# Kernel tuning notes

Measured on AMD Instinct MI355X. Metric: run time of the kernel, lower is better.

## Reference

```python
import jax, jax.numpy as jnp
import numpy as np

N_NODES = 100000
N_EDGES = 3200000
M = 24
HID = 32
OUT = 16


def neighbor_mean(feat, row, col, num_nodes):
    # sum features of source nodes into destination nodes, divide by in-degree
    sums = jax.ops.segment_sum(feat[row], col, num_segments=num_nodes)  # (N, F)
    deg = jax.ops.segment_sum(jnp.ones_like(col, dtype=feat.dtype), col, num_segments=num_nodes)
    return sums / jnp.clip(deg, 1.0)[:, None]


def sage_conv(x, row, col, num_nodes, w_l, b_l, w_r):
    # PyG SAGEConv(aggr='mean'): lin_l(mean_aggr) + lin_r(x); lin_r has no bias
    aggr = neighbor_mean(x, row, col, num_nodes)
    return aggr @ w_l.T + b_l + x @ w_r.T


def setup_inputs() -> dict:
    key = jax.random.key(0)
    ks = jax.random.split(key, 10)
    x_bin = jax.random.randint(ks[0], (N_NODES, M), 0, 2).astype(jnp.float32)
    edge_index = jax.random.randint(ks[1], (2, N_EDGES), 0, N_NODES).astype(jnp.int64)
    s = 0.1
    return {
        "x_bin": x_bin,
        "edge_index": edge_index,
        "w1l": s * jax.random.normal(ks[2], (HID, M), jnp.float32),
        "b1": s * jax.random.normal(ks[3], (HID,), jnp.float32),
        "w1r": s * jax.random.normal(ks[4], (HID, M), jnp.float32),
        "w2l": s * jax.random.normal(ks[5], (OUT, HID), jnp.float32),
        "b2": s * jax.random.normal(ks[6], (OUT,), jnp.float32),
        "w2r": s * jax.random.normal(ks[7], (OUT, HID), jnp.float32),
        "head_w": s * jax.random.normal(ks[8], (1, 3 * M + OUT), jnp.float32),
        "head_b": s * jax.random.normal(ks[9], (1,), jnp.float32),
    }


def reference(x_bin, edge_index, w1l, b1, w1r, w2l, b2, w2r, head_w, head_b):
    num_nodes = x_bin.shape[0]
    row, col = edge_index[0], edge_index[1]
    # explicit branch: [self markers | neighbor fraction | self * neighbor fraction]
    frac1 = neighbor_mean(x_bin, row, col, num_nodes)
    feats = jnp.concatenate([x_bin, frac1, x_bin * frac1], axis=1)  # (N, 3M)
    # GNN branch: SmallSAGE (dropout is identity at inference)
    h = jax.nn.relu(sage_conv(x_bin, row, col, num_nodes, w1l, b1, w1r))
    emb = jax.nn.relu(sage_conv(h, row, col, num_nodes, w2l, b2, w2r))  # (N, OUT)
    z = jnp.concatenate([feats, emb], axis=1)  # (N, 3M+OUT)
    yhat = (z @ head_w.T + head_b)[:, 0]  # (N,)
    return yhat, z
```

## Files before the change

### kernel.cpp

```cpp
#include <hip/hip_runtime.h>
#include <hip/hip_bf16.h>

#define MF 24
#define HIDF 32
#define OUTF 16
#define ZDIM 88
#define NPB 8
#define NPB2 32
#define SW1 28
#define SW2 36

#define NB 512
#define EB 8192
#define CAP 8192

union bf16x8 {
    float4 v;
    __hip_bfloat16 h[8];
};
union bf16x2u {
    unsigned int u;
    __hip_bfloat16 h[2];
};

__device__ __forceinline__ float ldw(const void* p, size_t i, bool bf16) {
    return bf16 ? __bfloat162float(((const __hip_bfloat16*)p)[i])
                : ((const float*)p)[i];
}

__device__ __forceinline__ bool detect_bf(const unsigned int* __restrict__ xw) {
    unsigned int w = xw[threadIdx.x & 63];
    return __ballot((w & 0xFFFFu) == 0x3F80u) != 0ull;
}
__device__ __forceinline__ bool detect_i64(const unsigned int* __restrict__ ew) {
    unsigned int w = ew[2 * (threadIdx.x & 63) + 1];
    return __popcll(__ballot(w == 0u)) >= 32;
}

__global__ __launch_bounds__(256) void k_histA(
    const void* __restrict__ x, unsigned int* __restrict__ xpack,
    const int* __restrict__ ei, int* __restrict__ counts,
    int nE, int N, int W) {
    const bool bf16 = detect_bf((const unsigned int*)x);
    const bool i64 = detect_i64((const unsigned int*)ei);

    for (int n = blockIdx.x * 256 + threadIdx.x; n < N; n += gridDim.x * 256) {
        unsigned int m = 0;
        if (bf16) {
            const float4* xr = reinterpret_cast<const float4*>(
                (const __hip_bfloat16*)x + (size_t)n * MF);
            bf16x8 u;
#pragma unroll
            for (int q = 0; q < 3; ++q) {
                u.v = xr[q];
#pragma unroll
                for (int i = 0; i < 8; ++i)
                    if (__bfloat162float(u.h[i]) != 0.f) m |= 1u << (q * 8 + i);
            }
        } else {
            const float* xr = (const float*)x + (size_t)n * MF;
#pragma unroll
            for (int k = 0; k < MF; ++k)
                if (xr[k] != 0.f) m |= 1u << k;
        }
        xpack[n] = m;
    }

    __shared__ int hist[NB];
    for (int i = threadIdx.x; i < NB; i += 256) hist[i] = 0;
    __syncthreads();
    size_t base = (size_t)blockIdx.x * EB;
    int m = nE - (int)base;
    if (m > EB) m = EB;
    for (int i = threadIdx.x; i < m; i += 256) {
        size_t e = base + i;
        int c = i64 ? ei[2 * ((size_t)nE + e)] : ei[(size_t)nE + e];
        if ((unsigned)c < (unsigned)N) atomicAdd(&hist[c / W], 1);
    }
    __syncthreads();
    for (int i = threadIdx.x; i < NB; i += 256)
        counts[(size_t)blockIdx.x * NB + i] = hist[i];
}

__global__ __launch_bounds__(1024) void k_colscan(int* __restrict__ counts,
                                                  int* __restrict__ colSum, int nBlk) {
    __shared__ int s[1024];
    int b = blockIdx.x, t = threadIdx.x;
    int v = (t < nBlk) ? counts[(size_t)t * NB + b] : 0;
    s[t] = v;
    __syncthreads();
    for (int off = 1; off < 1024; off <<= 1) {
        int y = (t >= off) ? s[t - off] : 0;
        __syncthreads();
        s[t] += y;
        __syncthreads();
    }
    if (t < nBlk) counts[(size_t)t * NB + b] = s[t] - v;
    if (t == 1023) colSum[b] = s[1023];
}

__global__ __launch_bounds__(1024) void k_bstart(const int* __restrict__ colSum,
                                                 int* __restrict__ bucketStart) {
    __shared__ int s[1024];
    int t = threadIdx.x;
    int v = (t < NB) ? colSum[t] : 0;
    s[t] = v;
    __syncthreads();
    for (int off = 1; off < 1024; off <<= 1) {
        int y = (t >= off) ? s[t - off] : 0;
        __syncthreads();
        s[t] += y;
        __syncthreads();
    }
    if (t < NB) bucketStart[t] = s[t] - v;
    if (t == NB - 1) bucketStart[NB] = s[t];
}

__global__ __launch_bounds__(256) void k_scatB(
    const int* __restrict__ ei, const int* __restrict__ counts,
    const int* __restrict__ colSum, const int* __restrict__ bucketStart,
    unsigned int* __restrict__ part, int nE, int N, int W, int nBlk) {
    const bool i64 = detect_i64((const unsigned int*)ei);
    __shared__ unsigned int rec[EB];
    __shared__ unsigned short bkt[EB];
    __shared__ int ldsStart[NB + 1];
    __shared__ int lcnt[NB];
    __shared__ int base2[NB];
    __shared__ int s256[256];
    const int t = threadIdx.x, blk = blockIdx.x;

    for (int b = t; b < NB; b += 256) {
        int pre = counts[(size_t)blk * NB + b];
        int nxt = (blk + 1 < nBlk) ? counts[(size_t)(blk + 1) * NB + b] : colSum[b];
        ldsStart[b] = nxt - pre;
        lcnt[b] = 0;
        base2[b] = bucketStart[b] + pre;
    }
    __syncthreads();

    int v0 = ldsStart[2 * t], v1 = ldsStart[2 * t + 1];
    int pairSum = v0 + v1;
    s256[t] = pairSum;
    __syncthreads();
    for (int off = 1; off < 256; off <<= 1) {
        int y = (t >= off) ? s256[t - off] : 0;
        __syncthreads();
        s256[t] += y;
        __syncthreads();
    }
    int base = s256[t] - pairSum;
    ldsStart[2 * t] = base;
    ldsStart[2 * t + 1] = base + v0;
    if (t == 255) ldsStart[NB] = base + pairSum;
    __syncthreads();
    for (int b = t; b < NB; b += 256) base2[b] -= ldsStart[b];
    __syncthreads();

    size_t eb = (size_t)blk * EB;
    int m = nE - (int)eb;
    if (m > EB) m = EB;
    for (int i = t; i < m; i += 256) {
        size_t e = eb + i;
        int r = i64 ? ei[2 * e] : ei[e];
        int c = i64 ? ei[2 * ((size_t)nE + e)] : ei[(size_t)nE + e];
        if ((unsigned)c < (unsigned)N) {
            int b = c / W;
            int ld = c - b * W;
            unsigned rr = ((unsigned)r < (unsigned)N) ? (unsigned)r : 0u;
            int pos = ldsStart[b] + atomicAdd(&lcnt[b], 1);
            rec[pos] = rr | ((unsigned)ld << 20);
            bkt[pos] = (unsigned short)b;
        }
    }
    __syncthreads();

    int total = ldsStart[NB];
    for (int i = t; i < total; i += 256) {
        int b = bkt[i];
        part[base2[b] + i] = rec[i];
    }
}

__global__ __launch_bounds__(256) void k_csrC(const int* __restrict__ bucketStart,
                                              unsigned int* __restrict__ part,
                                              int* __restrict__ degi,
                                              int* __restrict__ rowstart,
                                              int N, int W) {
    __shared__ unsigned int stage[CAP];
    __shared__ int hist[256];
    __shared__ int sc[256];
    __shared__ int cur[256];
    int b = blockIdx.x, t = threadIdx.x;
    int start = bucketStart[b];
    int bs = bucketStart[b + 1] - start;
    int node = b * W + t;

    hist[t] = 0;
    __syncthreads();

    if (bs > CAP) {
        if (t < W && node < N) { degi[node] = 0; rowstart[node] = start; }
        return;
    }

    for (int i = t; i < bs; i += 256) {
        unsigned int v = part[start + i];
        stage[i] = v;
        atomicAdd(&hist[v >> 20], 1);
    }
    __syncthreads();

    int v = hist[t];
    sc[t] = v;
    __syncthreads();
    for (int off = 1; off < 256; off <<= 1) {
        int y = (t >= off) ? sc[t - off] : 0;
        __syncthreads();
        sc[t] += y;
        __syncthreads();
    }
    int excl = sc[t] - v;
    if (t < W && node < N) {
        degi[node] = v;
        rowstart[node] = start + excl;
    }
    cur[t] = excl;
    __syncthreads();

    for (int i = t; i < bs; i += 256) {
        unsigned int v2 = stage[i];
        int pos = atomicAdd(&cur[v2 >> 20], 1);
        part[start + pos] = v2 & 0xFFFFFu;
    }
}

__device__ __forceinline__ unsigned tstage(unsigned x, unsigned y, unsigned M,
                                           int d, bool hi) {
    return x ^ (hi ? (((y >> d) ^ x) & M) : (((((x >> d) ^ y) & M)) << d));
}

__device__ __forceinline__ unsigned tcol(unsigned x, int lane) {
    unsigned y;
    y = (unsigned)__builtin_amdgcn_ds_swizzle((int)x, 0x401F);
    x = tstage(x, y, 0x0000FFFFu, 16, (lane & 16) != 0);
    y = (unsigned)__builtin_amdgcn_ds_swizzle((int)x, 0x201F);
    x = tstage(x, y, 0x00FF00FFu, 8, (lane & 8) != 0);
    y = (unsigned)__builtin_amdgcn_ds_swizzle((int)x, 0x101F);
    x = tstage(x, y, 0x0F0F0F0Fu, 4, (lane & 4) != 0);
    y = (unsigned)__builtin_amdgcn_ds_swizzle((int)x, 0x081F);
    x = tstage(x, y, 0x33333333u, 2, (lane & 2) != 0);
    y = (unsigned)__builtin_amdgcn_ds_swizzle((int)x, 0x041F);
    x = tstage(x, y, 0x55555555u, 1, (lane & 1) != 0);
    return x;
}

__global__ __launch_bounds__(256) void k_layer1(
    const void* __restrict__ x, const unsigned int* __restrict__ xpack,
    const int* __restrict__ degi, const int* __restrict__ rowstart,
    const unsigned int* __restrict__ srcs, void* __restrict__ out,
    const void* __restrict__ w1l, const void* __restrict__ b1,
    const void* __restrict__ w1r, const void* __restrict__ w2l,
    const void* __restrict__ b2, const void* __restrict__ w2r,
    const void* __restrict__ head_w,
    __hip_bfloat16* __restrict__ hl, __hip_bfloat16* __restrict__ st,
    float* __restrict__ ypart, int N) {
    const bool bf16 = detect_bf((const unsigned int*)x);
    __shared__ float swl[HIDF * SW1];
    __shared__ float swr[HIDF * SW1];
    __shared__ float sb[HIDF];
    __shared__ float s2l[OUTF * SW2];
    __shared__ float s2r[OUTF * SW2];
    __shared__ float sb2[OUTF];
    __shared__ float shw[3 * MF];
    __shared__ float fs[NPB][MF];
    __shared__ float hs[NPB][HIDF];
    for (int i = threadIdx.x; i < HIDF * MF; i += 256) {
        int j = i / MF, k = i - j * MF;
        swl[j * SW1 + k] = ldw(w1l, i, bf16);
        swr[j * SW1 + k] = ldw(w1r, i, bf16);
    }
    for (int i = threadIdx.x; i < OUTF * HIDF; i += 256) {
        int o = i >> 5, j = i & 31;
        s2l[o * SW2 + j] = ldw(w2l, i, bf16);
        s2r[o * SW2 + j] = ldw(w2r, i, bf16);
    }
    if (threadIdx.x < HIDF) sb[threadIdx.x] = ldw(b1, threadIdx.x, bf16);
    if (threadIdx.x < OUTF) sb2[threadIdx.x] = ldw(b2, threadIdx.x, bf16);
    if (threadIdx.x < 3 * MF) shw[threadIdx.x] = ldw(head_w, threadIdx.x, bf16);
    __syncthreads();

    const int lane = threadIdx.x & 31;
    const int wg = threadIdx.x >> 5;
    int node = blockIdx.x * NPB + wg;
    bool valid = node < N;

    int dg = 0, p0 = 0;
    unsigned int xpn = 0;
    if (valid) {
        dg = degi[node];
        p0 = rowstart[node];
        xpn = xpack[node];
    }

    int dgmax = dg;
#pragma unroll
    for (int off = 32; off > 0; off >>= 1)
        dgmax = max(dgmax, __shfl_xor(dgmax, off, 64));

    int cnt = 0;
    for (int base = 0; base < dgmax; base += 128) {
        unsigned int m0 = 0, m1 = 0, m2 = 0, m3 = 0;
        int e0 = base + lane;
        if (e0 < dg) m0 = xpack[srcs[p0 + e0]];
        if (e0 + 32 < dg) m1 = xpack[srcs[p0 + e0 + 32]];
        if (e0 + 64 < dg) m2 = xpack[srcs[p0 + e0 + 64]];
        if (e0 + 96 < dg) m3 = xpack[srcs[p0 + e0 + 96]];
        cnt += __popc(tcol(m0, lane));
        if (base + 32 < dgmax) cnt += __popc(tcol(m1, lane));
        if (base + 64 < dgmax) cnt += __popc(tcol(m2, lane));
        if (base + 96 < dgmax) cnt += __popc(tcol(m3, lane));
    }

    float inv = 1.f / fmaxf((float)dg, 1.f);
    float fv = (float)cnt * inv;
    float xv = (float)((xpn >> lane) & 1);

    float pc = 0.f;
    if (valid && lane < MF) {
        if (bf16) {
            __hip_bfloat16* z = (__hip_bfloat16*)out + N + (size_t)node * ZDIM;
            z[lane] = __float2bfloat16(xv);
            z[MF + lane] = __float2bfloat16(fv);
            z[2 * MF + lane] = __float2bfloat16(xv * fv);
        } else {
            float* z = (float*)out + N + (size_t)node * ZDIM;
            z[lane] = xv;
            z[MF + lane] = fv;
            z[2 * MF + lane] = xv * fv;
        }
        pc = xv * shw[lane] + fv * shw[MF + lane] + xv * fv * shw[2 * MF + lane];
    }

    if (lane < MF) fs[wg][lane] = fv;

    float fvk[MF];
    {
        const float4* fp = (const float4*)fs[wg];
#pragma unroll
        for (int q = 0; q < 6; ++q) {
            float4 f4 = fp[q];
            fvk[q * 4 + 0] = f4.x; fvk[q * 4 + 1] = f4.y;
            fvk[q * 4 + 2] = f4.z; fvk[q * 4 + 3] = f4.w;
        }
    }
    float wlv[MF], wrv[MF];
    {
        const float4* wl4 = (const float4*)(swl + lane * SW1);
        const float4* wr4 = (const float4*)(swr + lane * SW1);
#pragma unroll
        for (int q = 0; q < 6; ++q) {
            float4 a = wl4[q], b = wr4[q];
            wlv[q * 4 + 0] = a.x; wlv[q * 4 + 1] = a.y;
            wlv[q * 4 + 2] = a.z; wlv[q * 4 + 3] = a.w;
            wrv[q * 4 + 0] = b.x; wrv[q * 4 + 1] = b.y;
            wrv[q * 4 + 2] = b.z; wrv[q * 4 + 3] = b.w;
        }
    }
    float acc = sb[lane];
#pragma unroll
    for (int k = 0; k < MF; ++k) {
        acc = fmaf(fvk[k], wlv[k], acc);
        acc += ((xpn >> k) & 1u) ? wrv[k] : 0.f;
    }
    hs[wg][lane] = fmaxf(acc, 0.f);

#pragma unroll
    for (int off = 16; off > 0; off >>= 1) pc += __shfl_down(pc, off, 32);

    int o = lane & 15;
    int half = lane >> 4;
    const float4* wrow4 = (const float4*)((half ? s2r : s2l) + o * SW2);
    const float4* hp4 = (const float4*)hs[wg];
    float d = 0.f;
#pragma unroll
    for (int q = 0; q < 8; ++q) {
        float4 hq = hp4[q], wq = wrow4[q];
        d += hq.x * wq.x + hq.y * wq.y + hq.z * wq.z + hq.w * wq.w;
    }
    if (valid) {
        if (half == 0) hl[(size_t)node * OUTF + o] = __float2bfloat16(d);
        else st[(size_t)node * OUTF + o] = __float2bfloat16(d + sb2[o]);
        if (lane == 0) ypart[node] = pc;
    }
}

__global__ __launch_bounds__(256) void k_layer2(
    const void* __restrict__ x, const int* __restrict__ degi,
    const int* __restrict__ rowstart, const unsigned int* __restrict__ srcs,
    const __hip_bfloat16* __restrict__ hl, const __hip_bfloat16* __restrict__ st,
    const float* __restrict__ ypart, void* __restrict__ out,
    const void* __restrict__ head_w, const void* __restrict__ head_b, int N) {
    const bool bf16 = detect_bf((const unsigned int*)x);
    __shared__ float shw2[OUTF];
    __shared__ float shb;
    if (threadIdx.x < OUTF) shw2[threadIdx.x] = ldw(head_w, 3 * MF + threadIdx.x, bf16);
    if (threadIdx.x == 0) shb = ldw(head_b, 0, bf16);
    __syncthreads();

    int lane = threadIdx.x & 7;
    int g = threadIdx.x >> 3;
    int node = blockIdx.x * NPB2 + g;
    bool valid = node < N;

    int dg = 0, p0 = 0;
    if (valid) {
        dg = degi[node];
        p0 = rowstart[node];
    }
    const unsigned int* hlw = (const unsigned int*)hl;
    float s0 = 0.f, s1 = 0.f;
    int e = 0;
    for (; e + 4 <= dg; e += 4) {
        int a = srcs[p0 + e], b = srcs[p0 + e + 1];
        int c = srcs[p0 + e + 2], d = srcs[p0 + e + 3];
        bf16x2u ua, ub, uc, ud;
        ua.u = hlw[(size_t)a * 8 + lane];
        ub.u = hlw[(size_t)b * 8 + lane];
        uc.u = hlw[(size_t)c * 8 + lane];
        ud.u = hlw[(size_t)d * 8 + lane];
        s0 += (__bfloat162float(ua.h[0]) + __bfloat162float(ub.h[0])) +
              (__bfloat162float(uc.h[0]) + __bfloat162float(ud.h[0]));
        s1 += (__bfloat162float(ua.h[1]) + __bfloat162float(ub.h[1])) +
              (__bfloat162float(uc.h[1]) + __bfloat162float(ud.h[1]));
    }
    for (; e < dg; ++e) {
        bf16x2u ua;
        ua.u = hlw[(size_t)srcs[p0 + e] * 8 + lane];
        s0 += __bfloat162float(ua.h[0]);
        s1 += __bfloat162float(ua.h[1]);
    }

    float emb0 = 0.f, emb1 = 0.f;
    if (valid) {
        float inv = 1.f / fmaxf((float)dg, 1.f);
        bf16x2u us;
        us.u = ((const unsigned int*)st)[(size_t)node * 8 + lane];
        emb0 = fmaxf(s0 * inv + __bfloat162float(us.h[0]), 0.f);
        emb1 = fmaxf(s1 * inv + __bfloat162float(us.h[1]), 0.f);
        if (bf16) {
            __hip_bfloat16* z = (__hip_bfloat16*)out + N + (size_t)node * ZDIM;
            z[3 * MF + 2 * lane] = __float2bfloat16(emb0);
            z[3 * MF + 2 * lane + 1] = __float2bfloat16(emb1);
        } else {
            float* z = (float*)out + N + (size_t)node * ZDIM;
            z[3 * MF + 2 * lane] = emb0;
            z[3 * MF + 2 * lane + 1] = emb1;
        }
    }
    float part = emb0 * shw2[2 * lane] + emb1 * shw2[2 * lane + 1];
#pragma unroll
    for (int off = 4; off > 0; off >>= 1) part += __shfl_down(part, off, 8);
    if (valid && lane == 0) {
        float y = ypart[node] + part + shb;
        if (bf16) ((__hip_bfloat16*)out)[node] = __float2bfloat16(y);
        else ((float*)out)[node] = y;
    }
}

extern "C" void kernel_launch(void* const* d_in, const int* in_sizes, int n_in,
                              void* d_out, int out_size, void* d_ws, size_t ws_size,
                              hipStream_t stream) {
    const void* x = d_in[0];
    const int* ei = (const int*)d_in[1];
    const void* w1l = d_in[2];
    const void* b1 = d_in[3];
    const void* w1r = d_in[4];
    const void* w2l = d_in[5];
    const void* b2 = d_in[6];
    const void* w2r = d_in[7];
    const void* head_w = d_in[8];
    const void* head_b = d_in[9];

    const int N = in_sizes[0] / MF;
    const int nE = in_sizes[1] / 2;
    const int W = (N + NB - 1) / NB;
    const int nBlkA = (nE + EB - 1) / EB;

    if (N > NB * 256 || N > 131072 || nBlkA > 1024 ||
        (size_t)nBlkA * NB < (size_t)N || nE < 64) return;

    int* bucketStart = (int*)((char*)d_ws + 256);
    int* colSum = bucketStart + (NB + 1);
    int* degi = colSum + NB;
    int* rowstart = degi + N;
    int* counts = rowstart + N;
    unsigned int* part = (unsigned int*)(counts + (size_t)nBlkA * NB);
    unsigned int* xpack = part + nE;
    __hip_bfloat16* hl = (__hip_bfloat16*)(xpack + N);
    __hip_bfloat16* st = hl + (size_t)N * OUTF;
    float* ypart = (float*)counts;

    const size_t need = 256 +
        ((size_t)(NB + 1) + NB + 2 * (size_t)N + (size_t)nBlkA * NB +
         (size_t)nE + (size_t)N) * 4 + (size_t)N * OUTF * 2 * 2;
    if (ws_size < need) return;

    const int gb1 = (N + NPB - 1) / NPB;
    const int gb2 = (N + NPB2 - 1) / NPB2;
    k_histA<<<nBlkA, 256, 0, stream>>>(x, xpack, ei, counts, nE, N, W);
    k_colscan<<<NB, 1024, 0, stream>>>(counts, colSum, nBlkA);
    k_bstart<<<1, 1024, 0, stream>>>(colSum, bucketStart);
    k_scatB<<<nBlkA, 256, 0, stream>>>(ei, counts, colSum, bucketStart,
                                       part, nE, N, W, nBlkA);
    k_csrC<<<NB, 256, 0, stream>>>(bucketStart, part, degi, rowstart, N, W);
    k_layer1<<<gb1, 256, 0, stream>>>(x, xpack, degi, rowstart, part, d_out,
                                      w1l, b1, w1r, w2l, b2, w2r, head_w,
                                      hl, st, ypart, N);
    k_layer2<<<gb2, 256, 0, stream>>>(x, degi, rowstart, part, hl, st, ypart,
                                      d_out, head_w, head_b, N);
}
```

Before: 256.1 us.

## Vectorize edge loads, use reciprocal bucket division, halve edge block, loop layer1 nodes

The histogram and scatter kernels now load edge indices two at a time with int2/int4 vector loads and compute bucket indices with a multiply-high reciprocal instead of an integer divide. The edge block size drops from 8192 to 4096, doubling the number of partition blocks and the size of the counts array. k_layer1 now handles two node groups per block in a loop, which halves its grid and amortizes the weight staging into LDS. Together these aim to cut the overhead of the CSR build and the layer-1 setup, at the cost of more colscan work and fewer layer-1 blocks in flight.

```diff
diff --git a/kernel.cpp b/kernel.cpp
--- a/kernel.cpp
+++ b/kernel.cpp
@@ -6,12 +6,13 @@
 #define OUTF 16
 #define ZDIM 88
 #define NPB 8
+#define NREP 2
 #define NPB2 32
 #define SW1 28
 #define SW2 36
 
 #define NB 512
-#define EB 8192
+#define EB 4096
 #define CAP 8192
 
 union bf16x8 {
@@ -37,10 +38,17 @@
     return __popcll(__ballot(w == 0u)) >= 32;
 }
 
+__device__ __forceinline__ int bkt_of(int c, unsigned long long Wm) {
+    return (int)(((unsigned long long)(unsigned)c * Wm) >> 32);
+}
+
+#define HIST_EDGE(c_)                                                   \
+    if ((unsigned)(c_) < (unsigned)N) atomicAdd(&hist[bkt_of(c_, Wm)], 1);
+
 __global__ __launch_bounds__(256) void k_histA(
     const void* __restrict__ x, unsigned int* __restrict__ xpack,
     const int* __restrict__ ei, int* __restrict__ counts,
-    int nE, int N, int W) {
+    int nE, int N, unsigned long long Wm) {
     const bool bf16 = detect_bf((const unsigned int*)x);
     const bool i64 = detect_i64((const unsigned int*)ei);
 
@@ -72,10 +80,34 @@
     size_t base = (size_t)blockIdx.x * EB;
     int m = nE - (int)base;
     if (m > EB) m = EB;
-    for (int i = threadIdx.x; i < m; i += 256) {
-        size_t e = base + i;
-        int c = i64 ? ei[2 * ((size_t)nE + e)] : ei[(size_t)nE + e];
-        if ((unsigned)c < (unsigned)N) atomicAdd(&hist[c / W], 1);
+    if (!(nE & 1)) {
+        int nPair = m >> 1;
+        if (i64) {
+            const int4* cp = (const int4*)ei + (((size_t)nE + base) >> 1);
+            for (int j = threadIdx.x; j < nPair; j += 256) {
+                int4 c4 = cp[j];
+                HIST_EDGE(c4.x);
+                HIST_EDGE(c4.z);
+            }
+        } else {
+            const int2* cp = (const int2*)ei + (((size_t)nE + base) >> 1);
+            for (int j = threadIdx.x; j < nPair; j += 256) {
+                int2 c2 = cp[j];
+                HIST_EDGE(c2.x);
+                HIST_EDGE(c2.y);
+            }
+        }
+        for (int i = (nPair << 1) + threadIdx.x; i < m; i += 256) {
+            size_t e = base + i;
+            int c = i64 ? ei[2 * ((size_t)nE + e)] : ei[(size_t)nE + e];
+            HIST_EDGE(c);
+        }
+    } else {
+        for (int i = threadIdx.x; i < m; i += 256) {
+            size_t e = base + i;
+            int c = i64 ? ei[2 * ((size_t)nE + e)] : ei[(size_t)nE + e];
+            HIST_EDGE(c);
+        }
     }
     __syncthreads();
     for (int i = threadIdx.x; i < NB; i += 256)
@@ -116,10 +148,21 @@
     if (t == NB - 1) bucketStart[NB] = s[t];
 }
 
+#define SCAT_EDGE(r_, c_)                                               \
+    if ((unsigned)(c_) < (unsigned)N) {                                 \
+        int b_ = bkt_of(c_, Wm);                                        \
+        int ld_ = (c_) - b_ * W;                                        \
+        unsigned rr_ = ((unsigned)(r_) < (unsigned)N) ? (unsigned)(r_) : 0u; \
+        int pos_ = ldsStart[b_] + atomicAdd(&lcnt[b_], 1);              \
+        rec[pos_] = rr_ | ((unsigned)ld_ << 20);                        \
+        bkt[pos_] = (unsigned short)b_;                                 \
+    }
+
 __global__ __launch_bounds__(256) void k_scatB(
     const int* __restrict__ ei, const int* __restrict__ counts,
     const int* __restrict__ colSum, const int* __restrict__ bucketStart,
-    unsigned int* __restrict__ part, int nE, int N, int W, int nBlk) {
+    unsigned int* __restrict__ part, int nE, int N, int W,
+    unsigned long long Wm, int nBlk) {
     const bool i64 = detect_i64((const unsigned int*)ei);
     __shared__ unsigned int rec[EB];
     __shared__ unsigned short bkt[EB];
@@ -159,17 +202,39 @@
     size_t eb = (size_t)blk * EB;
     int m = nE - (int)eb;
     if (m > EB) m = EB;
-    for (int i = t; i < m; i += 256) {
-        size_t e = eb + i;
-        int r = i64 ? ei[2 * e] : ei[e];
-        int c = i64 ? ei[2 * ((size_t)nE + e)] : ei[(size_t)nE + e];
-        if ((unsigned)c < (unsigned)N) {
-            int b = c / W;
-            int ld = c - b * W;
-            unsigned rr = ((unsigned)r < (unsigned)N) ? (unsigned)r : 0u;
-            int pos = ldsStart[b] + atomicAdd(&lcnt[b], 1);
-            rec[pos] = rr | ((unsigned)ld << 20);
-            bkt[pos] = (unsigned short)b;
+    if (!(nE & 1)) {
+        int nPair = m >> 1;
+        if (i64) {
+            const int4* rp = (const int4*)ei + (eb >> 1);
+            const int4* cp = (const int4*)ei + (((size_t)nE + eb) >> 1);
+            for (int j = t; j < nPair; j += 256) {
+                int4 r4 = rp[j];
+                int4 c4 = cp[j];
+                SCAT_EDGE(r4.x, c4.x);
+                SCAT_EDGE(r4.z, c4.z);
+            }
+        } else {
+            const int2* rp = (const int2*)ei + (eb >> 1);
+            const int2* cp = (const int2*)ei + (((size_t)nE + eb) >> 1);
+            for (int j = t; j < nPair; j += 256) {
+                int2 r2 = rp[j];
+                int2 c2 = cp[j];
+                SCAT_EDGE(r2.x, c2.x);
+                SCAT_EDGE(r2.y, c2.y);
+            }
+        }
+        for (int i = (nPair << 1) + t; i < m; i += 256) {
+            size_t e = eb + i;
+            int r = i64 ? ei[2 * e] : ei[e];
+            int c = i64 ? ei[2 * ((size_t)nE + e)] : ei[(size_t)nE + e];
+            SCAT_EDGE(r, c);
+        }
+    } else {
+        for (int i = t; i < m; i += 256) {
+            size_t e = eb + i;
+            int r = i64 ? ei[2 * e] : ei[e];
+            int c = i64 ? ei[2 * ((size_t)nE + e)] : ei[(size_t)nE + e];
+            SCAT_EDGE(r, c);
         }
     }
     __syncthreads();
@@ -291,106 +356,110 @@
 
     const int lane = threadIdx.x & 31;
     const int wg = threadIdx.x >> 5;
-    int node = blockIdx.x * NPB + wg;
-    bool valid = node < N;
-
-    int dg = 0, p0 = 0;
-    unsigned int xpn = 0;
-    if (valid) {
-        dg = degi[node];
-        p0 = rowstart[node];
-        xpn = xpack[node];
-    }
-
-    int dgmax = dg;
-#pragma unroll
-    for (int off = 32; off > 0; off >>= 1)
-        dgmax = max(dgmax, __shfl_xor(dgmax, off, 64));
-
-    int cnt = 0;
-    for (int base = 0; base < dgmax; base += 128) {
-        unsigned int m0 = 0, m1 = 0, m2 = 0, m3 = 0;
-        int e0 = base + lane;
-        if (e0 < dg) m0 = xpack[srcs[p0 + e0]];
-        if (e0 + 32 < dg) m1 = xpack[srcs[p0 + e0 + 32]];
-        if (e0 + 64 < dg) m2 = xpack[srcs[p0 + e0 + 64]];
-        if (e0 + 96 < dg) m3 = xpack[srcs[p0 + e0 + 96]];
-        cnt += __popc(tcol(m0, lane));
-        if (base + 32 < dgmax) cnt += __popc(tcol(m1, lane));
-        if (base + 64 < dgmax) cnt += __popc(tcol(m2, lane));
-        if (base + 96 < dgmax) cnt += __popc(tcol(m3, lane));
-    }
-
-    float inv = 1.f / fmaxf((float)dg, 1.f);
-    float fv = (float)cnt * inv;
-    float xv = (float)((xpn >> lane) & 1);
-
-    float pc = 0.f;
-    if (valid && lane < MF) {
-        if (bf16) {
-            __hip_bfloat16* z = (__hip_bfloat16*)out + N + (size_t)node * ZDIM;
-            z[lane] = __float2bfloat16(xv);
-            z[MF + lane] = __float2bfloat16(fv);
-            z[2 * MF + lane] = __float2bfloat16(xv * fv);
-        } else {
-            float* z = (float*)out + N + (size_t)node * ZDIM;
-            z[lane] = xv;
-            z[MF + lane] = fv;
-            z[2 * MF + lane] = xv * fv;
-        }
-        pc = xv * shw[lane] + fv * shw[MF + lane] + xv * fv * shw[2 * MF + lane];
-    }
-
-    if (lane < MF) fs[wg][lane] = fv;
-
-    float fvk[MF];
-    {
-        const float4* fp = (const float4*)fs[wg];
-#pragma unroll
-        for (int q = 0; q < 6; ++q) {
-            float4 f4 = fp[q];
-            fvk[q * 4 + 0] = f4.x; fvk[q * 4 + 1] = f4.y;
-            fvk[q * 4 + 2] = f4.z; fvk[q * 4 + 3] = f4.w;
-        }
-    }
-    float wlv[MF], wrv[MF];
-    {
-        const float4* wl4 = (const float4*)(swl + lane * SW1);
-        const float4* wr4 = (const float4*)(swr + lane * SW1);
-#pragma unroll
-        for (int q = 0; q < 6; ++q) {
-            float4 a = wl4[q], b = wr4[q];
-            wlv[q * 4 + 0] = a.x; wlv[q * 4 + 1] = a.y;
-            wlv[q * 4 + 2] = a.z; wlv[q * 4 + 3] = a.w;
-            wrv[q * 4 + 0] = b.x; wrv[q * 4 + 1] = b.y;
-            wrv[q * 4 + 2] = b.z; wrv[q * 4 + 3] = b.w;
-        }
-    }
-    float acc = sb[lane];
-#pragma unroll
-    for (int k = 0; k < MF; ++k) {
-        acc = fmaf(fvk[k], wlv[k], acc);
-        acc += ((xpn >> k) & 1u) ? wrv[k] : 0.f;
-    }
-    hs[wg][lane] = fmaxf(acc, 0.f);
-
-#pragma unroll
-    for (int off = 16; off > 0; off >>= 1) pc += __shfl_down(pc, off, 32);
-
-    int o = lane & 15;
-    int half = lane >> 4;
-    const float4* wrow4 = (const float4*)((half ? s2r : s2l) + o * SW2);
-    const float4* hp4 = (const float4*)hs[wg];
-    float d = 0.f;
-#pragma unroll
-    for (int q = 0; q < 8; ++q) {
-        float4 hq = hp4[q], wq = wrow4[q];
-        d += hq.x * wq.x + hq.y * wq.y + hq.z * wq.z + hq.w * wq.w;
-    }
-    if (valid) {
-        if (half == 0) hl[(size_t)node * OUTF + o] = __float2bfloat16(d);
-        else st[(size_t)node * OUTF + o] = __float2bfloat16(d + sb2[o]);
-        if (lane == 0) ypart[node] = pc;
+
+#pragma unroll 1
+    for (int rep = 0; rep < NREP; ++rep) {
+        int node = blockIdx.x * (NPB * NREP) + rep * NPB + wg;
+        bool valid = node < N;
+
+        int dg = 0, p0 = 0;
+        unsigned int xpn = 0;
+        if (valid) {
+            dg = degi[node];
+            p0 = rowstart[node];
+            xpn = xpack[node];
+        }
+
+        int dgmax = dg;
+#pragma unroll
+        for (int off = 32; off > 0; off >>= 1)
+            dgmax = max(dgmax, __shfl_xor(dgmax, off, 64));
+
+        int cnt = 0;
+        for (int base = 0; base < dgmax; base += 128) {
+            unsigned int m0 = 0, m1 = 0, m2 = 0, m3 = 0;
+            int e0 = base + lane;
+            if (e0 < dg) m0 = xpack[srcs[p0 + e0]];
+            if (e0 + 32 < dg) m1 = xpack[srcs[p0 + e0 + 32]];
+            if (e0 + 64 < dg) m2 = xpack[srcs[p0 + e0 + 64]];
+            if (e0 + 96 < dg) m3 = xpack[srcs[p0 + e0 + 96]];
+            cnt += __popc(tcol(m0, lane));
+            if (base + 32 < dgmax) cnt += __popc(tcol(m1, lane));
+            if (base + 64 < dgmax) cnt += __popc(tcol(m2, lane));
+            if (base + 96 < dgmax) cnt += __popc(tcol(m3, lane));
+        }
+
+        float inv = 1.f / fmaxf((float)dg, 1.f);
+        float fv = (float)cnt * inv;
+        float xv = (float)((xpn >> lane) & 1);
+
+        float pc = 0.f;
+        if (valid && lane < MF) {
+            if (bf16) {
+                __hip_bfloat16* z = (__hip_bfloat16*)out + N + (size_t)node * ZDIM;
+                z[lane] = __float2bfloat16(xv);
+                z[MF + lane] = __float2bfloat16(fv);
+                z[2 * MF + lane] = __float2bfloat16(xv * fv);
+            } else {
+                float* z = (float*)out + N + (size_t)node * ZDIM;
+                z[lane] = xv;
+                z[MF + lane] = fv;
+                z[2 * MF + lane] = xv * fv;
+            }
+            pc = xv * shw[lane] + fv * shw[MF + lane] + xv * fv * shw[2 * MF + lane];
+        }
+
+        if (lane < MF) fs[wg][lane] = fv;
+
+        float fvk[MF];
+        {
+            const float4* fp = (const float4*)fs[wg];
+#pragma unroll
+            for (int q = 0; q < 6; ++q) {
+                float4 f4 = fp[q];
+                fvk[q * 4 + 0] = f4.x; fvk[q * 4 + 1] = f4.y;
+                fvk[q * 4 + 2] = f4.z; fvk[q * 4 + 3] = f4.w;
+            }
+        }
+        float wlv[MF], wrv[MF];
+        {
+            const float4* wl4 = (const float4*)(swl + lane * SW1);
+            const float4* wr4 = (const float4*)(swr + lane * SW1);
+#pragma unroll
+            for (int q = 0; q < 6; ++q) {
+                float4 a = wl4[q], b = wr4[q];
+                wlv[q * 4 + 0] = a.x; wlv[q * 4 + 1] = a.y;
+                wlv[q * 4 + 2] = a.z; wlv[q * 4 + 3] = a.w;
+                wrv[q * 4 + 0] = b.x; wrv[q * 4 + 1] = b.y;
+                wrv[q * 4 + 2] = b.z; wrv[q * 4 + 3] = b.w;
+            }
+        }
+        float acc = sb[lane];
+#pragma unroll
+        for (int k = 0; k < MF; ++k) {
+            acc = fmaf(fvk[k], wlv[k], acc);
+            acc += ((xpn >> k) & 1u) ? wrv[k] : 0.f;
+        }
+        hs[wg][lane] = fmaxf(acc, 0.f);
+
+#pragma unroll
+        for (int off = 16; off > 0; off >>= 1) pc += __shfl_down(pc, off, 32);
+
+        int o = lane & 15;
+        int half = lane >> 4;
+        const float4* wrow4 = (const float4*)((half ? s2r : s2l) + o * SW2);
+        const float4* hp4 = (const float4*)hs[wg];
+        float d = 0.f;
+#pragma unroll
+        for (int q = 0; q < 8; ++q) {
+            float4 hq = hp4[q], wq = wrow4[q];
+            d += hq.x * wq.x + hq.y * wq.y + hq.z * wq.z + hq.w * wq.w;
+        }
+        if (valid) {
+            if (half == 0) hl[(size_t)node * OUTF + o] = __float2bfloat16(d);
+            else st[(size_t)node * OUTF + o] = __float2bfloat16(d + sb2[o]);
+            if (lane == 0) ypart[node] = pc;
+        }
     }
 }
 
@@ -484,6 +553,7 @@
     const int N = in_sizes[0] / MF;
     const int nE = in_sizes[1] / 2;
     const int W = (N + NB - 1) / NB;
+    const unsigned long long Wm = (0x100000000ull / (unsigned)W) + 1;
     const int nBlkA = (nE + EB - 1) / EB;
 
     if (N > NB * 256 || N > 131072 || nBlkA > 1024 ||
@@ -505,13 +575,13 @@
          (size_t)nE + (size_t)N) * 4 + (size_t)N * OUTF * 2 * 2;
     if (ws_size < need) return;
 
-    const int gb1 = (N + NPB - 1) / NPB;
+    const int gb1 = (N + NPB * NREP - 1) / (NPB * NREP);
     const int gb2 = (N + NPB2 - 1) / NPB2;
-    k_histA<<<nBlkA, 256, 0, stream>>>(x, xpack, ei, counts, nE, N, W);
+    k_histA<<<nBlkA, 256, 0, stream>>>(x, xpack, ei, counts, nE, N, Wm);
     k_colscan<<<NB, 1024, 0, stream>>>(counts, colSum, nBlkA);
     k_bstart<<<1, 1024, 0, stream>>>(colSum, bucketStart);
     k_scatB<<<nBlkA, 256, 0, stream>>>(ei, counts, colSum, bucketStart,
-                                       part, nE, N, W, nBlkA);
+                                       part, nE, N, W, Wm, nBlkA);
     k_csrC<<<NB, 256, 0, stream>>>(bucketStart, part, degi, rowstart, N, W);
     k_layer1<<<gb1, 256, 0, stream>>>(x, xpack, degi, rowstart, part, d_out,
                                       w1l, b1, w1r, w2l, b2, w2r, head_w,
```

Measured after the change: 255.8 us. Within noise of the previous version (-0.1%).
